# Kernel tuning notes

Hardware: AMD Instinct MI355X
Metric: run time of the kernel (lower is better)

The kernel has to match this reference:

```python
import jax, jax.numpy as jnp
import numpy as np

B, S, E, H = 2, 2048, 1024, 16
Dh = E // H
LN_EPS = 1e-5


def setup_inputs() -> dict:
    key = jax.random.key(0)
    ks = jax.random.split(key, 12)
    std = 1.0 / np.sqrt(E)
    inp = {
        "query": jax.random.normal(ks[0], (B, S, E), jnp.float32),
        "key":   jax.random.normal(ks[1], (B, S, E), jnp.float32),
        "value": jax.random.normal(ks[2], (B, S, E), jnp.float32),
        # True = masked. Causal mask so every row keeps >=1 valid entry.
        "mask": jnp.broadcast_to(jnp.triu(jnp.ones((S, S), bool), k=1), (B, S, S)),
        # per-head QKV projections, stacked: weight [H, Dh, E] (torch Linear layout), bias [H, Dh]
        "Wq_w": jax.random.uniform(ks[3], (H, Dh, E), jnp.float32, -std, std),
        "Wq_b": jax.random.uniform(ks[4], (H, Dh), jnp.float32, -std, std),
        "Wk_w": jax.random.uniform(ks[5], (H, Dh, E), jnp.float32, -std, std),
        "Wk_b": jax.random.uniform(ks[6], (H, Dh), jnp.float32, -std, std),
        "Wv_w": jax.random.uniform(ks[7], (H, Dh, E), jnp.float32, -std, std),
        "Wv_b": jax.random.uniform(ks[8], (H, Dh), jnp.float32, -std, std),
        # output projection [E, E] (torch layout: out = x @ W.T + b)
        "out_w": jax.random.uniform(ks[9], (E, E), jnp.float32, -std, std),
        "out_b": jax.random.uniform(ks[10], (E,), jnp.float32, -std, std),
        "ln_g": jnp.ones((E,), jnp.float32),
        "ln_b": jnp.zeros((E,), jnp.float32),
    }
    return inp


def reference(query, key, value, mask, Wq_w, Wq_b, Wk_w, Wk_b, Wv_w, Wv_b, out_w, out_b, ln_g, ln_b):
    # per-head projections (batched over heads): [B,S,E] x [H,Dh,E] -> [B,H,S,Dh]
    q = jnp.einsum('bse,hde->bhsd', query, Wq_w) + Wq_b[None, :, None, :]
    k = jnp.einsum('bse,hde->bhsd', key,   Wk_w) + Wk_b[None, :, None, :]
    v = jnp.einsum('bse,hde->bhsd', value, Wv_w) + Wv_b[None, :, None, :]
    scale = 1.0 / np.sqrt(Dh).astype(np.float32)
    scores = jnp.einsum('bhsd,bhtd->bhst', q, k) * scale  # [B,H,S,S]
    scores = jnp.where(mask[:, None, :, :], -jnp.inf, scores)
    probs = jax.nn.softmax(scores, axis=-1)  # dropout p=0 (eval)
    ctx = jnp.einsum('bhst,bhtd->bhsd', probs, v)  # [B,H,S,Dh]
    att = ctx.transpose(0, 2, 1, 3).reshape(query.shape[0], query.shape[1], -1)  # concat heads [B,S,E]
    proj = att @ out_w.T + out_b  # dropout p=0
    x = query + proj  # residual
    mu = jnp.mean(x, axis=-1, keepdims=True)
    var = jnp.mean(jnp.square(x - mu), axis=-1, keepdims=True)
    return (x - mu) * jax.lax.rsqrt(var + LN_EPS) * ln_g + ln_b
```

## Files before the change

kernel.cpp:

```cpp
#include <hip/hip_runtime.h>
#include <stdint.h>

#define B_ 2
#define S_ 2048
#define E_ 1024
#define H_ 16
#define DH 64
#define M_TOT (B_*S_)

typedef short s16x8 __attribute__((ext_vector_type(8)));
typedef float f32x4 __attribute__((ext_vector_type(4)));
typedef unsigned int u32;
typedef unsigned short u16;

union V8 { uint4 u; s16x8 v; };

__device__ __forceinline__ u32 fbits(float f){ union{float f;u32 i;}x; x.f=f; return x.i; }
__device__ __forceinline__ u32 prround(float f){ return fbits(f)+0x8000u; }
__device__ __forceinline__ u16 f2bf(float f){ return (u16)(prround(f)>>16); }
__device__ __forceinline__ u32 permpack(u32 hi,u32 lo){ return __builtin_amdgcn_perm(hi,lo,0x07060302u); }
__device__ __forceinline__ uint4 pack8r(const float4 a, const float4 b){
    uint4 p;
    p.x = permpack(prround(a.y),prround(a.x));
    p.y = permpack(prround(a.w),prround(a.z));
    p.z = permpack(prround(b.y),prround(b.x));
    p.w = permpack(prround(b.w),prround(b.z));
    return p;
}
__device__ __forceinline__ float exp2_fast(float x){ float r; asm("v_exp_f32 %0, %1":"=v"(r):"v"(x)); return r; }

typedef const __attribute__((address_space(1))) u32* gas_t;
typedef __attribute__((address_space(3))) u32* las_t;
#define GLDS16(gp, lp) __builtin_amdgcn_global_load_lds((gas_t)(gp), (las_t)(lp), 16, 0, 0)

#define MFMA16(a,b,c) __builtin_amdgcn_mfma_f32_16x16x32_bf16((a),(b),(c),0,0,0)

__global__ __launch_bounds__(256) void cvtw(
    const float* __restrict__ w0, const float* __restrict__ w1, const float* __restrict__ w2,
    u16* __restrict__ dst, int n4)
{
    const int z = blockIdx.y;
    const float* s = (z==0)?w0:(z==1)?w1:w2;
    u16* d = dst + (size_t)z*E_*E_;
    int i = blockIdx.x*256 + threadIdx.x;
    const int stride = gridDim.x*256;
    for (; i<n4; i+=stride){
        float4 v = ((const float4*)s)[i];
        uint2 p;
        p.x = permpack(prround(v.y),prround(v.x));
        p.y = permpack(prround(v.w),prround(v.z));
        ((uint2*)d)[i] = p;
    }
}
__global__ __launch_bounds__(256) void cvt1(
    const float* __restrict__ s, u16* __restrict__ d, int n4)
{
    int i = blockIdx.x*256 + threadIdx.x;
    const int stride = gridDim.x*256;
    for (; i<n4; i+=stride){
        float4 v = ((const float4*)s)[i];
        uint2 p;
        p.x = permpack(prround(v.y),prround(v.x));
        p.y = permpack(prround(v.w),prround(v.z));
        ((uint2*)d)[i] = p;
    }
}
__global__ __launch_bounds__(256) void cvtx(
    const float* __restrict__ x0, const float* __restrict__ x1, const float* __restrict__ x2,
    u16* __restrict__ d0, u16* __restrict__ d1, u16* __restrict__ d2, int n4)
{
    const int z = blockIdx.y;
    const float* s = (z==0)?x0:(z==1)?x1:x2;
    u16* d = (z==0)?d0:(z==1)?d1:d2;
    int i = blockIdx.x*256 + threadIdx.x;
    const int stride = gridDim.x*256;
    for (; i<n4; i+=stride){
        float4 v = ((const float4*)s)[i];
        uint2 p;
        p.x = permpack(prround(v.y),prround(v.x));
        p.y = permpack(prround(v.w),prround(v.z));
        ((uint2*)d)[i] = p;
    }
}

__global__ __launch_bounds__(256,3) void qkv128(
    const float* __restrict__ xv,
    const u16* __restrict__ xqb, const u16* __restrict__ xkb, const u16* __restrict__ xvb,
    const u16* __restrict__ Wb,
    const float* __restrict__ bq, const float* __restrict__ bk, const float* __restrict__ bv,
    u16* __restrict__ oq, u16* __restrict__ ok_, u16* __restrict__ ovt)
{
    const int bid = blockIdx.x;
    const int c = bid & 7;
    const int tdec = bid >> 3;
    const int n = tdec & 7;
    const int g = ((tdec >> 3) << 3) + c;
    const int m = g & 31, z = g >> 5;

    const u16* W = Wb + (size_t)z*E_*E_;
    const float* bia = (z==0)?bq:(z==1)?bk:bv;
    const float scale = (z==0)? 0.125f*1.44269504f : 1.0f;

    __shared__ __align__(16) u16 As[3][128*32];
    __shared__ __align__(16) u16 Bs[3][128*32];

    const int tid = threadIdx.x;
    const int wid = tid>>6, lane = tid&63;
    const int lrow = lane&15, quad = lane>>4;
    const int mb = m*128, nb = n*128;
    const int wm = (wid>>1)*64, wn = (wid&1)*64;
    const int srow = lane>>2, skq = lane&3;

    f32x4 acc[4][4] = {};
    const u16*  Wn = W + (size_t)nb*E_;

    auto stageB = [&](u16* Bd, int kt){
        const int k0 = kt*32;
#pragma unroll
        for (int i=0;i<2;i++){
            const int rb = wid*32 + i*16;
            GLDS16(Wn + (size_t)(rb+srow)*E_ + k0 + ((skq^(srow&3))<<3), Bd + rb*32);
        }
    };

    const u16* Abf = (z==0)? xqb : (z==1)? xkb : xvb;

    if (Abf){
        const u16* Am = Abf + (size_t)mb*E_;
        auto stageA = [&](u16* Ad, int kt){
            const int k0 = kt*32;
#pragma unroll
            for (int i=0;i<2;i++){
                const int rb = wid*32 + i*16;
                GLDS16(Am + (size_t)(rb+srow)*E_ + k0 + ((skq^(srow&3))<<3), Ad + rb*32);
            }
        };
        stageA(As[0], 0); stageB(Bs[0], 0);
        stageA(As[1], 1); stageB(Bs[1], 1);

        int tc = 0;
#pragma unroll 1
        for (int kt=0; kt<32; ++kt){
            const int ts = (kt+2 < 32) ? kt+2 : 31;
            const int tn = (tc+2 >= 3) ? tc-1 : tc+2;
            asm volatile("s_waitcnt vmcnt(4) lgkmcnt(0)" ::: "memory");
            __builtin_amdgcn_s_barrier();
            __builtin_amdgcn_sched_barrier(0);

            const u16* Ad = As[tc];
            const u16* Bd = Bs[tc];
            const int fq_ = (quad^(lrow&3))<<3;
            s16x8 a0 = *(const s16x8*)&Ad[(wm+ 0+lrow)*32 + fq_];
            s16x8 a1 = *(const s16x8*)&Ad[(wm+16+lrow)*32 + fq_];
            s16x8 a2 = *(const s16x8*)&Ad[(wm+32+lrow)*32 + fq_];
            s16x8 a3 = *(const s16x8*)&Ad[(wm+48+lrow)*32 + fq_];
            s16x8 b0 = *(const s16x8*)&Bd[(wn+ 0+lrow)*32 + fq_];
            s16x8 b1 = *(const s16x8*)&Bd[(wn+16+lrow)*32 + fq_];
            s16x8 b2 = *(const s16x8*)&Bd[(wn+32+lrow)*32 + fq_];
            s16x8 b3 = *(const s16x8*)&Bd[(wn+48+lrow)*32 + fq_];
            __builtin_amdgcn_sched_barrier(0);
            stageA(As[tn], ts);
            stageB(Bs[tn], ts);
            __builtin_amdgcn_sched_barrier(0);
            __builtin_amdgcn_s_setprio(1);
            acc[0][0] = MFMA16(a0, b0, acc[0][0]);
            acc[0][1] = MFMA16(a0, b1, acc[0][1]);
            acc[0][2] = MFMA16(a0, b2, acc[0][2]);
            acc[0][3] = MFMA16(a0, b3, acc[0][3]);
            acc[1][0] = MFMA16(a1, b0, acc[1][0]);
            acc[1][1] = MFMA16(a1, b1, acc[1][1]);
            acc[1][2] = MFMA16(a1, b2, acc[1][2]);
            acc[1][3] = MFMA16(a1, b3, acc[1][3]);
            acc[2][0] = MFMA16(a2, b0, acc[2][0]);
            acc[2][1] = MFMA16(a2, b1, acc[2][1]);
            acc[2][2] = MFMA16(a2, b2, acc[2][2]);
            acc[2][3] = MFMA16(a2, b3, acc[2][3]);
            acc[3][0] = MFMA16(a3, b0, acc[3][0]);
            acc[3][1] = MFMA16(a3, b1, acc[3][1]);
            acc[3][2] = MFMA16(a3, b2, acc[3][2]);
            acc[3][3] = MFMA16(a3, b3, acc[3][3]);
            __builtin_amdgcn_s_setprio(0);
            tc = (tc+1==3)?0:tc+1;
        }
        asm volatile("s_waitcnt vmcnt(0) lgkmcnt(0)" ::: "memory");
    } else {
        const int arow = wid*32 + (lane>>1);
        const int akh  = lane&1;
        const int ag0  = akh*2;
        const int asw  = arow&3;
        const float* Xrow = xv + (size_t)(mb+arow)*E_ + akh*16;

        float4 arA0, arA1, arA2, arA3;
        float4 arB0, arB1, arB2, arB3;

#define QKV_ISSUEA(KT, AR) do {                                   \
        const float* xp_ = Xrow + ((KT)<<5);                      \
        AR##0 = *(const float4*)(xp_    );                        \
        AR##1 = *(const float4*)(xp_ + 4);                        \
        AR##2 = *(const float4*)(xp_ + 8);                        \
        AR##3 = *(const float4*)(xp_ +12);                        \
    } while(0)

#define QKV_WRITEA(AD, AR) do {                                   \
        const uint4 w0_ = pack8r(AR##0, AR##1);                   \
        const uint4 w1_ = pack8r(AR##2, AR##3);                   \
        *(uint4*)&(AD)[arow*32 + (((ag0  )^asw)<<3)] = w0_;       \
        *(uint4*)&(AD)[arow*32 + (((ag0+1)^asw)<<3)] = w1_;       \
    } while(0)

#define QKV_ITER(KT, TC, ARC, ARN) do {                                       \
        const int ts_ = ((KT)+2 < 32) ? (KT)+2 : 31;                          \
        const int tw_ = ((TC)+1==3)?0:(TC)+1;                                 \
        const int tn_ = (tw_+1==3)?0:tw_+1;                                   \
        const u16* Ad_ = As[TC];                                              \
        const u16* Bd_ = Bs[TC];                                              \
        asm volatile("s_waitcnt vmcnt(6) lgkmcnt(0)" ::: "memory");           \
        __builtin_amdgcn_s_barrier();                                         \
        __builtin_amdgcn_sched_barrier(0);                                    \
        const int fq_ = (quad^(lrow&3))<<3;                                   \
        s16x8 a0 = *(const s16x8*)&Ad_[(wm+ 0+lrow)*32 + fq_];                \
        s16x8 a1 = *(const s16x8*)&Ad_[(wm+16+lrow)*32 + fq_];                \
        s16x8 a2 = *(const s16x8*)&Ad_[(wm+32+lrow)*32 + fq_];                \
        s16x8 a3 = *(const s16x8*)&Ad_[(wm+48+lrow)*32 + fq_];                \
        s16x8 b0 = *(const s16x8*)&Bd_[(wn+ 0+lrow)*32 + fq_];                \
        s16x8 b1 = *(const s16x8*)&Bd_[(wn+16+lrow)*32 + fq_];                \
        s16x8 b2 = *(const s16x8*)&Bd_[(wn+32+lrow)*32 + fq_];                \
        s16x8 b3 = *(const s16x8*)&Bd_[(wn+48+lrow)*32 + fq_];                \
        __builtin_amdgcn_sched_barrier(0);                                    \
        QKV_ISSUEA(ts_, ARN);                                                 \
        __builtin_amdgcn_sched_barrier(0);                                    \
        stageB(Bs[tn_], ts_);                                                 \
        __builtin_amdgcn_sched_barrier(0);                                    \
        __builtin_amdgcn_s_setprio(1);                                        \
        acc[0][0] = MFMA16(a0, b0, acc[0][0]);                                \
        acc[0][1] = MFMA16(a0, b1, acc[0][1]);                                \
        acc[0][2] = MFMA16(a0, b2, acc[0][2]);                                \
        acc[0][3] = MFMA16(a0, b3, acc[0][3]);                                \
        acc[1][0] = MFMA16(a1, b0, acc[1][0]);                                \
        acc[1][1] = MFMA16(a1, b1, acc[1][1]);                                \
        acc[1][2] = MFMA16(a1, b2, acc[1][2]);                                \
        acc[1][3] = MFMA16(a1, b3, acc[1][3]);                                \
        __builtin_amdgcn_s_setprio(0);                                        \
        QKV_WRITEA(As[tw_], ARC);                                             \
        __builtin_amdgcn_s_setprio(1);                                        \
        acc[2][0] = MFMA16(a2, b0, acc[2][0]);                                \
        acc[2][1] = MFMA16(a2, b1, acc[2][1]);                                \
        acc[2][2] = MFMA16(a2, b2, acc[2][2]);                                \
        acc[2][3] = MFMA16(a2, b3, acc[2][3]);                                \
        acc[3][0] = MFMA16(a3, b0, acc[3][0]);                                \
        acc[3][1] = MFMA16(a3, b1, acc[3][1]);                                \
        acc[3][2] = MFMA16(a3, b2, acc[3][2]);                                \
        acc[3][3] = MFMA16(a3, b3, acc[3][3]);                                \
        __builtin_amdgcn_s_setprio(0);                                        \
    } while(0)

        QKV_ISSUEA(0, arA);
        stageB(Bs[0], 0);
        QKV_WRITEA(As[0], arA);
        QKV_ISSUEA(1, arA);
        stageB(Bs[1], 1);

        int tc = 0;
#pragma unroll 1
        for (int k2=0; k2<16; ++k2){
            const int kt0 = k2*2;
            QKV_ITER(kt0,   tc, arA, arB);
            tc = (tc+1==3)?0:tc+1;
            QKV_ITER(kt0+1, tc, arB, arA);
            tc = (tc+1==3)?0:tc+1;
        }
        asm volatile("s_waitcnt vmcnt(0) lgkmcnt(0)" ::: "memory");
#undef QKV_ITER
#undef QKV_WRITEA
#undef QKV_ISSUEA
    }

    if (z < 2){
        u16* O = (z==0)?oq:ok_;
#pragma unroll
        for (int ci=0;ci<4;ci++){
            const int nn = nb+wn+ci*16+lrow;
            const float bval = bia[nn];
            const int h = nn>>6, d = nn&63;
#pragma unroll
            for (int mi=0;mi<4;mi++){
#pragma unroll
                for (int r=0;r<4;r++){
                    const int mm = mb+wm+mi*16+quad*4+r;
                    const int bb = mm>>11, s = mm&(S_-1);
                    O[(((size_t)(bb*H_+h))*S_+s)*DH + d] = f2bf((acc[mi][ci][r]+bval)*scale);
                }
            }
        }
    } else {
#pragma unroll
        for (int ci=0;ci<4;ci++){
            const int nn = nb+wn+ci*16+lrow;
            const float bval = bia[nn];
            const int h = nn>>6, d = nn&63;
#pragma unroll
            for (int mi=0;mi<4;mi++){
                const int m0 = mb+wm+mi*16+quad*4;
                const int bb = m0>>11, s0 = m0&(S_-1);
                uint2 pk;
                pk.x = permpack(prround(acc[mi][ci][1]+bval), prround(acc[mi][ci][0]+bval));
                pk.y = permpack(prround(acc[mi][ci][3]+bval), prround(acc[mi][ci][2]+bval));
                *(uint2*)&ovt[(((size_t)(bb*H_+h))*DH + d)*S_ + s0] = pk;
            }
        }
    }
}

__global__ __launch_bounds__(256) void attn(
    const u16* __restrict__ q_ws, const u16* __restrict__ k_ws,
    const u16* __restrict__ vt_ws, u16* __restrict__ att)
{
    const int bid = blockIdx.x;
    const int c8 = bid & 7;
    const int t = bid >> 3;
    const int p = t & 15;
    const int bh = ((t >> 4) << 3) + c8;
    const int b = bh>>4, h = bh&15;

    const u16* Qb = q_ws + (size_t)bh*S_*DH;
    const u16* Kb = k_ws + (size_t)bh*S_*DH;
    const u16* VT = vt_ws + (size_t)bh*DH*S_;

    __shared__ __align__(16) u16 Ks0[64*64];
    __shared__ __align__(16) u16 Ks1[64*64];
    __shared__ __align__(16) u16 Vt0[64*64];
    __shared__ __align__(16) u16 Vt1[64*64];
    __shared__ __align__(16) u16 Ps[4][16*64];

    const int tid = threadIdx.x;
    const int wid = tid>>6, lane = tid&63;
    const int lrow = lane&15, quad = lane>>4;
    u16* Pw = Ps[wid];

    const int srw = lane>>3;
    const int scs = lane&7;
    const int sgc = scs ^ srw;

    auto stageKV = [&](u16* Kd, u16* Vd, int t0){
#pragma unroll
        for (int g2=0; g2<2; g2++){
            const int rg = wid*16 + g2*8 + srw;
            GLDS16(Kb + (size_t)(t0+rg)*DH + (sgc<<3), Kd + (wid*16+g2*8)*64);
            GLDS16(VT + (size_t)rg*S_ + t0 + (sgc<<3), Vd + (wid*16+g2*8)*64);
        }
    };

    for (int ph=0; ph<2; ph++){
        const int qi = ph ? (31-p) : p;
        const int qb = qi<<6;

        s16x8 qf[2];
#pragma unroll
        for (int ch=0;ch<2;ch++)
            qf[ch] = *(const s16x8*)&Qb[(size_t)(qb+wid*16+lrow)*DH + ch*32 + quad*8];

        f32x4 o[4] = {};
        float l_lane = 0.f;
        const int qglob = qb + wid*16 + lrow;
        const int ntile = qi + 1;

        auto computeTile = [&](const u16* Kd, const u16* Vd, int t0, bool diag){
            f32x4 st[4] = {};
#pragma unroll
            for (int tt=0;tt<4;tt++){
                const int tr = tt*16+lrow;
#pragma unroll
                for (int ch=0;ch<2;ch++){
                    const int slot = (ch*4+quad) ^ (lrow&7);
                    const s16x8 kf = *(const s16x8*)&Kd[tr*64 + slot*8];
                    st[tt] = __builtin_amdgcn_mfma_f32_16x16x32_bf16(kf, qf[ch], st[tt],0,0,0);
                }
            }
            if (diag){
#pragma unroll
                for (int tt=0;tt<4;tt++){
                    const int tg = t0 + tt*16 + quad*4;
#pragma unroll
                    for (int r=0;r<4;r++)
                        if (tg + r > qglob) st[tt][r] = -1e30f;
                }
            }
#pragma unroll
            for (int tt=0;tt<4;tt++){
                const float p0 = exp2_fast(st[tt][0]);
                const float p1 = exp2_fast(st[tt][1]);
                const float p2 = exp2_fast(st[tt][2]);
                const float p3 = exp2_fast(st[tt][3]);
                l_lane += (p0+p1)+(p2+p3);
                const int tc = tt*2 + (quad>>1);
                const int ts = tc ^ (lrow&7);
                const int a0 = lrow*64 + ts*8 + (quad&1)*4;
                *(u32*)&Pw[a0]   = permpack(prround(p1),prround(p0));
                *(u32*)&Pw[a0+2] = permpack(prround(p3),prround(p2));
            }
            s16x8 pb[2];
#pragma unroll
            for (int ch=0;ch<2;ch++){
                const int slot = (ch*4+quad) ^ (lrow&7);
                pb[ch] = *(const s16x8*)&Pw[lrow*64 + slot*8];
            }
#pragma unroll
            for (int cc=0;cc<4;cc++){
                const int vr = cc*16+lrow;
#pragma unroll
                for (int ch=0;ch<2;ch++){
                    const int slot = (ch*4+quad) ^ (lrow&7);
                    const s16x8 vf = *(const s16x8*)&Vd[vr*64 + slot*8];
                    o[cc] = __builtin_amdgcn_mfma_f32_16x16x32_bf16(vf, pb[ch], o[cc],0,0,0);
                }
            }
        };

        __syncthreads();
        stageKV(Ks0, Vt0, 0);
        for (int ti=0; ; ti+=2){
            __syncthreads();
            if (ti+1 < ntile) stageKV(Ks1, Vt1, (ti+1)<<6);
            computeTile(Ks0, Vt0, ti<<6, ti==ntile-1);
            if (ti+1 >= ntile) break;
            __syncthreads();
            if (ti+2 < ntile) stageKV(Ks0, Vt0, (ti+2)<<6);
            computeTile(Ks1, Vt1, (ti+1)<<6, ti+1==ntile-1);
            if (ti+2 >= ntile) break;
        }

        float s = l_lane;
        s += __shfl_xor(s, 16, 64);
        s += __shfl_xor(s, 32, 64);
        const float rl = 1.0f/s;

#pragma unroll
        for (int cc=0;cc<4;cc++){
            uint2 pk;
            pk.x = permpack(prround(o[cc][1]*rl), prround(o[cc][0]*rl));
            pk.y = permpack(prround(o[cc][3]*rl), prround(o[cc][2]*rl));
            *(uint2*)&att[(size_t)(b*S_ + qglob)*E_ + h*DH + cc*16 + quad*4] = pk;
        }
    }
}

__global__ __launch_bounds__(256) void oproj128(
    const u16* __restrict__ A, const u16* __restrict__ W, const float* __restrict__ bias,
    const float* __restrict__ resid, float* __restrict__ out)
{
    const int bid = blockIdx.x;
    const int c = bid & 7;
    const int tdec = bid >> 3;
    const int n = tdec & 15;
    const int m = ((tdec >> 4) << 3) + c;

    __shared__ __align__(16) u16 As[3][128*32];
    __shared__ __align__(16) u16 Bs[3][64*32];

    const int tid = threadIdx.x;
    const int wid = tid>>6, lane = tid&63;
    const int lrow = lane&15, quad = lane>>4;
    const int mb = m*128, nb = n*64;
    const int srow = lane>>2, skq = lane&3;

    f32x4 acc[2][4] = {};
    const u16* Ab = A + (size_t)mb*E_;
    const u16* Wn = W + (size_t)nb*E_;

    auto stage = [&](u16* Ad, u16* Bd, int kt){
        const int k0 = kt*32;
        const int kc = (skq^(srow&3))<<3;
#pragma unroll
        for (int i=0;i<2;i++){
            const int rb = wid*32 + i*16;
            GLDS16(Ab + (size_t)(rb+srow)*E_ + k0 + kc, Ad + rb*32);
        }
        GLDS16(Wn + (size_t)(wid*16+srow)*E_ + k0 + kc, Bd + (wid*16)*32);
    };

    stage(As[0], Bs[0], 0);
    stage(As[1], Bs[1], 1);

    int tc = 0, tn = 2;
#pragma unroll 1
    for (int kt=0; kt<32; ++kt){
        const int ts = (kt+2 < 32) ? kt+2 : 31;
        asm volatile("s_waitcnt vmcnt(3) lgkmcnt(0)" ::: "memory");
        __builtin_amdgcn_s_barrier();
        __builtin_amdgcn_sched_barrier(0);

        const u16* Ad = As[tc];
        const u16* Bd = Bs[tc];
        const int sw = lrow&3;
        s16x8 a0 = *(const s16x8*)&Ad[(wid*32+ 0+lrow)*32 + ((quad^sw)<<3)];
        s16x8 a1 = *(const s16x8*)&Ad[(wid*32+16+lrow)*32 + ((quad^sw)<<3)];
        s16x8 b0 = *(const s16x8*)&Bd[( 0+lrow)*32 + ((quad^sw)<<3)];
        s16x8 b1 = *(const s16x8*)&Bd[(16+lrow)*32 + ((quad^sw)<<3)];
        s16x8 b2 = *(const s16x8*)&Bd[(32+lrow)*32 + ((quad^sw)<<3)];
        s16x8 b3 = *(const s16x8*)&Bd[(48+lrow)*32 + ((quad^sw)<<3)];
        stage(As[tn], Bs[tn], ts);
        __builtin_amdgcn_s_setprio(1);
        acc[0][0] = MFMA16(a0, b0, acc[0][0]);
        acc[0][1] = MFMA16(a0, b1, acc[0][1]);
        acc[0][2] = MFMA16(a0, b2, acc[0][2]);
        acc[0][3] = MFMA16(a0, b3, acc[0][3]);
        acc[1][0] = MFMA16(a1, b0, acc[1][0]);
        acc[1][1] = MFMA16(a1, b1, acc[1][1]);
        acc[1][2] = MFMA16(a1, b2, acc[1][2]);
        acc[1][3] = MFMA16(a1, b3, acc[1][3]);
        __builtin_amdgcn_s_setprio(0);
        tc = (tc+1==3)?0:tc+1;
        tn = (tn+1==3)?0:tn+1;
    }
    asm volatile("s_waitcnt vmcnt(0)" ::: "memory");

#pragma unroll
    for (int ci=0;ci<4;ci++){
        const int nn = nb+ci*16+lrow;
        const float bval = bias[nn];
#pragma unroll
        for (int mi=0;mi<2;mi++){
#pragma unroll
            for (int r=0;r<4;r++){
                const int mm = mb+wid*32+mi*16+quad*4+r;
                out[(size_t)mm*E_+nn] = acc[mi][ci][r] + bval + resid[(size_t)mm*E_+nn];
            }
        }
    }
}

__global__ __launch_bounds__(256) void ln_k(
    const float* __restrict__ xin, const float* __restrict__ lg,
    const float* __restrict__ lb, float* __restrict__ out)
{
    const int row = blockIdx.x;
    const int tid = threadIdx.x;
    const int wid = tid>>6, lane = tid&63;
    const float* xr = xin + (size_t)row*E_;

    float x[4];
    float s = 0.f;
#pragma unroll
    for (int i=0;i<4;i++){ const int e = i*256+tid; x[i] = xr[e]; s += x[i]; }
    __shared__ float red[8];
#pragma unroll
    for (int off=32; off>0; off>>=1) s += __shfl_xor(s, off, 64);
    if (lane==0) red[wid] = s;
    __syncthreads();
    const float mu = (red[0]+red[1]+red[2]+red[3]) * (1.f/E_);

    float v = 0.f;
#pragma unroll
    for (int i=0;i<4;i++){ const float d = x[i]-mu; v += d*d; }
#pragma unroll
    for (int off=32; off>0; off>>=1) v += __shfl_xor(v, off, 64);
    if (lane==0) red[wid+4] = v;
    __syncthreads();
    const float var = (red[4]+red[5]+red[6]+red[7]) * (1.f/E_);
    const float rs = rsqrtf(var + 1e-5f);

#pragma unroll
    for (int i=0;i<4;i++){
        const int e = i*256+tid;
        out[(size_t)row*E_+e] = (x[i]-mu)*rs*lg[e] + lb[e];
    }
}

extern "C" void kernel_launch(void* const* d_in, const int* in_sizes, int n_in,
                              void* d_out, int out_size, void* d_ws, size_t ws_size,
                              hipStream_t stream) {
    const float* q_in = (const float*)d_in[0];
    const float* k_in = (const float*)d_in[1];
    const float* v_in = (const float*)d_in[2];
    const float* wq = (const float*)d_in[4];
    const float* bq = (const float*)d_in[5];
    const float* wk = (const float*)d_in[6];
    const float* bk = (const float*)d_in[7];
    const float* wv = (const float*)d_in[8];
    const float* bv = (const float*)d_in[9];
    const float* ow = (const float*)d_in[10];
    const float* ob = (const float*)d_in[11];
    const float* lg = (const float*)d_in[12];
    const float* lb = (const float*)d_in[13];
    float* out = (float*)d_out;

    char* ws = (char*)d_ws;
    const size_t MB = (size_t)1<<20;
    u16* q_ws  = (u16*)(ws);
    u16* k_ws  = (u16*)(ws +  8*MB);
    u16* vt_ws = (u16*)(ws + 16*MB);
    u16* att   = (u16*)(ws + 24*MB);
    u16* Wbf   = (u16*)(ws + 24*MB);
    u16* owbf  = (u16*)(ws + 16*MB);
    float* proj = (float*)ws;

    u16* xqbf = (u16*)out;
    u16* xkbf = (u16*)((char*)out + 8*MB);
    u16* xvbf = (ws_size >= 40*MB) ? (u16*)(ws + 32*MB) : (u16*)0;

    cvtw<<<dim3(512,3), 256, 0, stream>>>(wq, wk, wv, Wbf, (E_*E_)/4);
    cvtx<<<dim3(1024, xvbf?3:2), 256, 0, stream>>>(
        q_in, k_in, v_in, xqbf, xkbf, xvbf, (M_TOT*E_)/4);
    qkv128<<<dim3(768), 256, 0, stream>>>(
        v_in, xqbf, xkbf, xvbf, Wbf, bq, bk, bv, q_ws, k_ws, vt_ws);
    attn<<<dim3(512), 256, 0, stream>>>(q_ws, k_ws, vt_ws, att);
    cvt1<<<dim3(1024), 256, 0, stream>>>(ow, owbf, (E_*E_)/4);
    oproj128<<<dim3(512), 256, 0, stream>>>(att, owbf, ob, q_in, proj);
    ln_k<<<dim3(M_TOT), 256, 0, stream>>>(proj, lg, lb, out);
}
```

Before: 241.2 us.

## Split attention KV range into two halves with separate reduction kernel

Adds an attn2 kernel that launches twice as many blocks, each taking every other KV tile of the causal range and writing unnormalized fp32 partial outputs and row sums. A new attn_red kernel sums the two halves, normalizes, and converts to bf16. All fp32-to-bf16 conversions are also merged into one launch. The aim is better GPU occupancy and fewer launches. The cost is about 32MB of extra fp32 partial traffic, and the path runs only when the workspace is at least 80MB.

```diff
diff --git a/kernel.cpp b/kernel.cpp
--- a/kernel.cpp
+++ b/kernel.cpp
@@ -72,6 +72,30 @@
     const int z = blockIdx.y;
     const float* s = (z==0)?x0:(z==1)?x1:x2;
     u16* d = (z==0)?d0:(z==1)?d1:d2;
+    int i = blockIdx.x*256 + threadIdx.x;
+    const int stride = gridDim.x*256;
+    for (; i<n4; i+=stride){
+        float4 v = ((const float4*)s)[i];
+        uint2 p;
+        p.x = permpack(prround(v.y),prround(v.x));
+        p.y = permpack(prround(v.w),prround(v.z));
+        ((uint2*)d)[i] = p;
+    }
+}
+__global__ __launch_bounds__(256) void cvtall(
+    const float* __restrict__ w0, const float* __restrict__ w1, const float* __restrict__ w2,
+    const float* __restrict__ ow,
+    const float* __restrict__ x0, const float* __restrict__ x1, const float* __restrict__ x2,
+    u16* __restrict__ wbf, u16* __restrict__ owbf,
+    u16* __restrict__ dq, u16* __restrict__ dk, u16* __restrict__ dv)
+{
+    const int z = blockIdx.y;
+    const float* s;
+    u16* d;
+    int n4;
+    if (z < 3){ s = (z==0)?w0:(z==1)?w1:w2; d = wbf + (size_t)z*E_*E_; n4 = (E_*E_)/4; }
+    else if (z == 3){ s = ow; d = owbf; n4 = (E_*E_)/4; }
+    else { s = (z==4)?x0:(z==5)?x1:x2; d = (z==4)?dq:(z==5)?dk:dv; n4 = (M_TOT*E_)/4; }
     int i = blockIdx.x*256 + threadIdx.x;
     const int stride = gridDim.x*256;
     for (; i<n4; i+=stride){
@@ -311,6 +335,168 @@
     }
 }
 
+__global__ __launch_bounds__(256,4) void attn2(
+    const u16* __restrict__ q_ws, const u16* __restrict__ k_ws,
+    const u16* __restrict__ vt_ws, float* __restrict__ opart,
+    float* __restrict__ lpart)
+{
+    const int bid = blockIdx.x;
+    const int c8 = bid & 7;
+    const int t = bid >> 3;
+    const int p = t & 15;
+    const int half = (t >> 4) & 1;
+    const int bh = ((t >> 5) << 3) + c8;
+    const int b = bh>>4, h = bh&15;
+
+    const u16* Qb = q_ws + (size_t)bh*S_*DH;
+    const u16* Kb = k_ws + (size_t)bh*S_*DH;
+    const u16* VT = vt_ws + (size_t)bh*DH*S_;
+
+    __shared__ __align__(16) u16 Ks0[64*64];
+    __shared__ __align__(16) u16 Ks1[64*64];
+    __shared__ __align__(16) u16 Vt0[64*64];
+    __shared__ __align__(16) u16 Vt1[64*64];
+    __shared__ __align__(16) u16 Ps[4][16*64];
+
+    const int tid = threadIdx.x;
+    const int wid = tid>>6, lane = tid&63;
+    const int lrow = lane&15, quad = lane>>4;
+    u16* Pw = Ps[wid];
+
+    const int srw = lane>>3;
+    const int scs = lane&7;
+    const int sgc = scs ^ srw;
+
+    auto stageKV = [&](u16* Kd, u16* Vd, int t0){
+#pragma unroll
+        for (int g2=0; g2<2; g2++){
+            const int rg = wid*16 + g2*8 + srw;
+            GLDS16(Kb + (size_t)(t0+rg)*DH + (sgc<<3), Kd + (wid*16+g2*8)*64);
+            GLDS16(VT + (size_t)rg*S_ + t0 + (sgc<<3), Vd + (wid*16+g2*8)*64);
+        }
+    };
+
+    for (int ph=0; ph<2; ph++){
+        const int qi = ph ? (31-p) : p;
+        const int qb = qi<<6;
+        const int nt = (qi >= half) ? (((qi - half) >> 1) + 1) : 0;
+
+        s16x8 qf[2];
+#pragma unroll
+        for (int ch=0;ch<2;ch++)
+            qf[ch] = *(const s16x8*)&Qb[(size_t)(qb+wid*16+lrow)*DH + ch*32 + quad*8];
+
+        f32x4 o[4] = {};
+        float l_lane = 0.f;
+        const int qglob = qb + wid*16 + lrow;
+
+        auto computeTile = [&](const u16* Kd, const u16* Vd, int t0, bool diag){
+            f32x4 st[4] = {};
+#pragma unroll
+            for (int tt=0;tt<4;tt++){
+                const int tr = tt*16+lrow;
+#pragma unroll
+                for (int ch=0;ch<2;ch++){
+                    const int slot = (ch*4+quad) ^ (lrow&7);
+                    const s16x8 kf = *(const s16x8*)&Kd[tr*64 + slot*8];
+                    st[tt] = __builtin_amdgcn_mfma_f32_16x16x32_bf16(kf, qf[ch], st[tt],0,0,0);
+                }
+            }
+            if (diag){
+#pragma unroll
+                for (int tt=0;tt<4;tt++){
+                    const int tg = t0 + tt*16 + quad*4;
+#pragma unroll
+                    for (int r=0;r<4;r++)
+                        if (tg + r > qglob) st[tt][r] = -1e30f;
+                }
+            }
+#pragma unroll
+            for (int tt=0;tt<4;tt++){
+                const float p0 = exp2_fast(st[tt][0]);
+                const float p1 = exp2_fast(st[tt][1]);
+                const float p2 = exp2_fast(st[tt][2]);
+                const float p3 = exp2_fast(st[tt][3]);
+                l_lane += (p0+p1)+(p2+p3);
+                const int tc = tt*2 + (quad>>1);
+                const int ts = tc ^ (lrow&7);
+                const int a0 = lrow*64 + ts*8 + (quad&1)*4;
+                *(u32*)&Pw[a0]   = permpack(prround(p1),prround(p0));
+                *(u32*)&Pw[a0+2] = permpack(prround(p3),prround(p2));
+            }
+            s16x8 pb[2];
+#pragma unroll
+            for (int ch=0;ch<2;ch++){
+                const int slot = (ch*4+quad) ^ (lrow&7);
+                pb[ch] = *(const s16x8*)&Pw[lrow*64 + slot*8];
+            }
+#pragma unroll
+            for (int cc=0;cc<4;cc++){
+                const int vr = cc*16+lrow;
+#pragma unroll
+                for (int ch=0;ch<2;ch++){
+                    const int slot = (ch*4+quad) ^ (lrow&7);
+                    const s16x8 vf = *(const s16x8*)&Vd[vr*64 + slot*8];
+                    o[cc] = __builtin_amdgcn_mfma_f32_16x16x32_bf16(vf, pb[ch], o[cc],0,0,0);
+                }
+            }
+        };
+
+        __syncthreads();
+        if (nt > 0){
+            stageKV(Ks0, Vt0, half<<6);
+            for (int i=0; ; i+=2){
+                __syncthreads();
+                if (i+1 < nt) stageKV(Ks1, Vt1, (half + 2*(i+1))<<6);
+                { const int tile = half + 2*i;
+                  computeTile(Ks0, Vt0, tile<<6, tile==qi); }
+                if (i+1 >= nt) break;
+                __syncthreads();
+                if (i+2 < nt) stageKV(Ks0, Vt0, (half + 2*(i+2))<<6);
+                { const int tile = half + 2*(i+1);
+                  computeTile(Ks1, Vt1, tile<<6, tile==qi); }
+                if (i+2 >= nt) break;
+            }
+        }
+
+        float s = l_lane;
+        s += __shfl_xor(s, 16, 64);
+        s += __shfl_xor(s, 32, 64);
+        if (quad == 0)
+            lpart[(size_t)half*(B_*H_*S_) + (size_t)bh*S_ + qglob] = s;
+
+        float* od = opart + (size_t)half*((size_t)M_TOT*E_)
+                  + ((size_t)(b*S_ + qglob))*E_ + h*DH;
+#pragma unroll
+        for (int cc=0;cc<4;cc++)
+            *(f32x4*)&od[cc*16 + quad*4] = o[cc];
+    }
+}
+
+__global__ __launch_bounds__(256) void attn_red(
+    const float* __restrict__ op, const float* __restrict__ lp,
+    u16* __restrict__ att)
+{
+    const int n4 = (M_TOT*E_)/4;
+    int i = blockIdx.x*256 + threadIdx.x;
+    const int stride = gridDim.x*256;
+    const float* op1 = op + (size_t)M_TOT*E_;
+    for (; i<n4; i+=stride){
+        float4 a = ((const float4*)op)[i];
+        float4 c = ((const float4*)op1)[i];
+        const int e0 = i*4;
+        const int r = e0 >> 10;
+        const int h = (e0 >> 6) & 15;
+        const int bb = r >> 11, s = r & (S_-1);
+        const size_t lidx = ((size_t)(bb*H_ + h))*S_ + s;
+        const float rl = 1.0f/(lp[lidx] + lp[(size_t)(B_*H_*S_) + lidx]);
+        uint2 pk;
+        pk.x = permpack(prround((a.y+c.y)*rl), prround((a.x+c.x)*rl));
+        pk.y = permpack(prround((a.w+c.w)*rl), prround((a.z+c.z)*rl));
+        ((uint2*)att)[i] = pk;
+    }
+}
+
 __global__ __launch_bounds__(256) void attn(
     const u16* __restrict__ q_ws, const u16* __restrict__ k_ws,
     const u16* __restrict__ vt_ws, u16* __restrict__ att)
@@ -591,20 +777,37 @@
     u16* vt_ws = (u16*)(ws + 16*MB);
     u16* att   = (u16*)(ws + 24*MB);
     u16* Wbf   = (u16*)(ws + 24*MB);
-    u16* owbf  = (u16*)(ws + 16*MB);
     float* proj = (float*)ws;
 
     u16* xqbf = (u16*)out;
     u16* xkbf = (u16*)((char*)out + 8*MB);
-    u16* xvbf = (ws_size >= 40*MB) ? (u16*)(ws + 32*MB) : (u16*)0;
-
-    cvtw<<<dim3(512,3), 256, 0, stream>>>(wq, wk, wv, Wbf, (E_*E_)/4);
-    cvtx<<<dim3(1024, xvbf?3:2), 256, 0, stream>>>(
-        q_in, k_in, v_in, xqbf, xkbf, xvbf, (M_TOT*E_)/4);
-    qkv128<<<dim3(768), 256, 0, stream>>>(
-        v_in, xqbf, xkbf, xvbf, Wbf, bq, bk, bv, q_ws, k_ws, vt_ws);
-    attn<<<dim3(512), 256, 0, stream>>>(q_ws, k_ws, vt_ws, att);
-    cvt1<<<dim3(1024), 256, 0, stream>>>(ow, owbf, (E_*E_)/4);
-    oproj128<<<dim3(512), 256, 0, stream>>>(att, owbf, ob, q_in, proj);
-    ln_k<<<dim3(M_TOT), 256, 0, stream>>>(proj, lg, lb, out);
-}
+
+    if (ws_size >= 80*MB){
+        u16*   xvbf  = (u16*)(ws + 32*MB);
+        float* opart = (float*)(ws + 40*MB);
+        float* lpart = (float*)(ws + 72*MB);
+        u16*   owbf  = (u16*)(ws + 73*MB);
+
+        cvtall<<<dim3(1024,7), 256, 0, stream>>>(
+            wq, wk, wv, ow, q_in, k_in, v_in, Wbf, owbf, xqbf, xkbf, xvbf);
+        qkv128<<<dim3(768), 256, 0, stream>>>(
+            v_in, xqbf, xkbf, xvbf, Wbf, bq, bk, bv, q_ws, k_ws, vt_ws);
+        attn2<<<dim3(1024), 256, 0, stream>>>(q_ws, k_ws, vt_ws, opart, lpart);
+        attn_red<<<dim3(2048), 256, 0, stream>>>(opart, lpart, att);
+        oproj128<<<dim3(512), 256, 0, stream>>>(att, owbf, ob, q_in, proj);
+        ln_k<<<dim3(M_TOT), 256, 0, stream>>>(proj, lg, lb, out);
+    } else {
+        u16* owbf = (u16*)(ws + 16*MB);
+        u16* xvbf = (ws_size >= 40*MB) ? (u16*)(ws + 32*MB) : (u16*)0;
+
+        cvtw<<<dim3(512,3), 256, 0, stream>>>(wq, wk, wv, Wbf, (E_*E_)/4);
+        cvtx<<<dim3(1024, xvbf?3:2), 256, 0, stream>>>(
+            q_in, k_in, v_in, xqbf, xkbf, xvbf, (M_TOT*E_)/4);
+        qkv128<<<dim3(768), 256, 0, stream>>>(
+            v_in, xqbf, xkbf, xvbf, Wbf, bq, bk, bv, q_ws, k_ws, vt_ws);
+        attn<<<dim3(512), 256, 0, stream>>>(q_ws, k_ws, vt_ws, att);
+        cvt1<<<dim3(1024), 256, 0, stream>>>(ow, owbf, (E_*E_)/4);
+        oproj128<<<dim3(512), 256, 0, stream>>>(att, owbf, ob, q_in, proj);
+        ln_k<<<dim3(M_TOT), 256, 0, stream>>>(proj, lg, lb, out);
+    }
+}
```

Result: no change. 243.6 us (+1.0%).
